# Optimization experiments

Measured on AMD Instinct MI355X. Metric: run time of the kernel, lower is better.

Reference implementation:

```python
import jax, jax.numpy as jnp
import numpy as np
from jax import lax

# STP parameters hard-coded in TFSTP.__init__ (stpPara)
U0 = 0.15        # u0
D_CONST = 0.05 * 20   # D = 1.0
F_CONST = 0.5 * 20    # F = 10.0
F_SMALL = 0.15        # f
R0 = 1.0


def _spike2interval(spk_bool):
    """Vectorized version of TFSTP.spike2interval.
    spk_bool: [T,H,W] bool. Returns isi [T,H,W] float32 with inf where undefined.
    For consecutive spikes s_k < s_{k+1}: isi[s_k+1 : s_{k+1}+1] = s_{k+1} - s_k.
    Equivalently isi[t] = next_spike_at_or_after(t) - last_spike_strictly_before(t).
    """
    T = spk_bool.shape[0]
    idx = jnp.arange(T, dtype=jnp.int32)[:, None, None]
    BIG = jnp.int32(T + 1)
    # last spike time <= t (running max of spike indices)
    prev_incl = lax.associative_scan(jnp.maximum, jnp.where(spk_bool, idx, -1), axis=0)
    # last spike time strictly < t (shift by one)
    prev_strict = jnp.concatenate(
        [jnp.full_like(prev_incl[:1], -1), prev_incl[:-1]], axis=0)
    # first spike time >= t (reverse running min)
    nxt = lax.associative_scan(jnp.minimum, jnp.where(spk_bool, idx, BIG),
                               axis=0, reverse=True)
    valid = (prev_strict >= 0) & (nxt < BIG)
    return jnp.where(valid, (nxt - prev_strict).astype(jnp.float32), jnp.inf)


def setup_inputs() -> dict:
    key = jax.random.key(0)
    T, H, W = 400, 250, 400
    spikes = jax.random.randint(key, (1, T, H, W), 0, 2).astype(jnp.float32)
    return {"spikes": spikes}


def reference(spikes):
    spk = spikes[0] > 0                    # [T,H,W] bool
    T, H, W = spk.shape
    half = T // 2                          # forward() breaks at t == T/2

    isi = _spike2interval(spk)             # [T,H,W]
    isi0 = isi[0]                          # prev_isi is fixed to intervals[0]

    R_init = jnp.full((H, W), R0, dtype=jnp.float32)
    u_init = jnp.full((H, W), U0, dtype=jnp.float32)

    def step(carry, xs):
        R, u = carry
        isi_t, spk_t = xs
        # update_idx = (isi_t != isi0) & (spk_t == 0) | (isi_t == 1)
        mask = ((isi_t != isi0) & (~spk_t)) | (isi_t == 1.0)
        exp_D = jnp.exp(-isi_t / D_CONST)   # exp(-inf)=0, discarded by mask
        exp_F = jnp.exp(-isi_t / F_CONST)
        R_new = jnp.where(mask, 1.0 - (1.0 - R * (1.0 - u)) * exp_D, R)
        u_new = jnp.where(mask, U0 + (u + F_SMALL * (1.0 - u) - U0) * exp_F, u)
        return (R_new, u_new), None

    # only the state at t = T//2 contributes to the output
    (R, u), _ = lax.scan(step, (R_init, u_init),
                         (isi[1:half + 1], spk[1:half + 1]))

    rho_u = -1.0 / (F_CONST * jnp.log(
        (u - U0) / (F_CONST - U0 + u * (1.0 - F_SMALL))))
    rho_R = -1.0 / (D_CONST * jnp.log(
        (1.0 - R) / (1.0 - R * (1.0 - u))))
    img = rho_u + rho_R

    mn, mx = img.min(), img.max()
    denom = jnp.where(mx == mn, 1.0, mx - mn)
    img = jnp.where(mx != mn, (img - mn) / denom, img)
    return img[None, None]  # [1,1,H,W]
```

## Files before the change

### kernel.cpp

```cpp
#include <hip/hip_runtime.h>
#include <math.h>

namespace {
constexpr int   T_STEPS = 400;
constexpr int   HALF    = 200;
constexpr int   NPIX    = 250 * 400;
constexpr int   CHUNK   = 32;
constexpr int   BLOCK   = 64;
constexpr int   NBLK    = (NPIX + BLOCK - 1) / BLOCK;
constexpr int   NORM_BLOCK = 256;
constexpr int   NORM_NBLK  = (NPIX + NORM_BLOCK - 1) / NORM_BLOCK;
constexpr float U0 = 0.15f;
}

__device__ __forceinline__ void apply_segment(float& R, float& u, int d, int n) {
  const float dd = (float)d;
  const float eD = expf(-dd);
  const float eF = expf(-(dd / 10.0f));
  for (int k = 0; k < n; ++k) {
    const float Rn = 1.0f - (1.0f - R * (1.0f - u)) * eD;
    const float un = U0 + (u + 0.15f * (1.0f - u) - U0) * eF;
    R = Rn; u = un;
  }
}

__device__ __forceinline__ void proc_mask(unsigned mask, int t0, int& prev,
                                          float& R, float& u, bool& done) {
  if (done) return;
  while (mask) {
    const int i = __builtin_ctz(mask);
    mask &= mask - 1u;
    const int t = t0 + i;
    if (prev >= 0) {
      const int d = t - prev;
      const int n = (t <= HALF) ? ((d == 1) ? 1 : (d - 1)) : (HALF - prev);
      apply_segment(R, u, d, n);
    }
    prev = t;
    if (t >= HALF) { done = true; return; }
  }
}

__global__ __launch_bounds__(BLOCK) void stp_compute(
    const float* __restrict__ spikes, float* __restrict__ img,
    float* __restrict__ pmin, float* __restrict__ pmax) {
  const int  p      = blockIdx.x * BLOCK + threadIdx.x;
  const bool active = (p < NPIX);
  const float* __restrict__ sp = spikes + (active ? p : (NPIX - 1));

  bool  done = !active;
  int   prev = -1;
  float R = 1.0f, u = U0;

  auto loadc = [&](float (&buf)[CHUNK], int c) {
#pragma unroll
    for (int i = 0; i < CHUNK; ++i) {
      const unsigned idx = (unsigned)(c * CHUNK + i) * (unsigned)NPIX;
      buf[i] = sp[idx];
    }
  };
  auto maskof = [&](const float (&buf)[CHUNK]) -> unsigned {
    unsigned m = 0u;
#pragma unroll
    for (int i = 0; i < CHUNK; ++i) m |= (buf[i] > 0.0f) ? (1u << i) : 0u;
    return m;
  };

  float va[CHUNK], vb[CHUNK];
  loadc(va, 0);
  loadc(vb, 1);
  unsigned m;
  m = maskof(va); loadc(va, 2); proc_mask(m, 0 * CHUNK, prev, R, u, done);
  m = maskof(vb); loadc(vb, 3); proc_mask(m, 1 * CHUNK, prev, R, u, done);
  m = maskof(va); loadc(va, 4); proc_mask(m, 2 * CHUNK, prev, R, u, done);
  m = maskof(vb); loadc(vb, 5); proc_mask(m, 3 * CHUNK, prev, R, u, done);
  m = maskof(va); loadc(va, 6); proc_mask(m, 4 * CHUNK, prev, R, u, done);
  m = maskof(vb);               proc_mask(m, 5 * CHUNK, prev, R, u, done);
  m = maskof(va);               proc_mask(m, 6 * CHUNK, prev, R, u, done);

  for (int c = 7; c <= (T_STEPS - 1) / CHUNK; ++c) {
    if (__all((int)done)) break;
    unsigned mt = 0u;
#pragma unroll
    for (int i = 0; i < CHUNK; ++i) {
      const int t = c * CHUNK + i;
      float v = 0.0f;
      if (t < T_STEPS) v = sp[(unsigned)t * (unsigned)NPIX];
      mt |= (v > 0.0f) ? (1u << i) : 0u;
    }
    proc_mask(mt, c * CHUNK, prev, R, u, done);
  }

  float val = 0.0f;
  if (active) {
    const float lu = logf((u - U0) / (10.0f - U0 + u * 0.85f));
    const float lR = logf((1.0f - R) / (1.0f - R * (1.0f - u)));
    val = (-1.0f / (10.0f * lu)) + (-1.0f / lR);
    img[p] = val;
  }

  float vmin = active ? val : INFINITY;
  float vmax = active ? val : -INFINITY;
#pragma unroll
  for (int off = 32; off > 0; off >>= 1) {
    vmin = fminf(vmin, __shfl_down(vmin, off, 64));
    vmax = fmaxf(vmax, __shfl_down(vmax, off, 64));
  }
  if (threadIdx.x == 0) {
    pmin[blockIdx.x] = vmin;
    pmax[blockIdx.x] = vmax;
  }
}

__global__ __launch_bounds__(512) void reduce_minmax(
    const float* __restrict__ pmin, const float* __restrict__ pmax,
    float* __restrict__ mm) {
  float vmin = INFINITY, vmax = -INFINITY;
  for (int i = threadIdx.x; i < NBLK; i += 512) {
    vmin = fminf(vmin, pmin[i]);
    vmax = fmaxf(vmax, pmax[i]);
  }
#pragma unroll
  for (int off = 32; off > 0; off >>= 1) {
    vmin = fminf(vmin, __shfl_down(vmin, off, 64));
    vmax = fmaxf(vmax, __shfl_down(vmax, off, 64));
  }
  __shared__ float smin[8], smax[8];
  const int lane = threadIdx.x & 63, wid = threadIdx.x >> 6;
  if (lane == 0) { smin[wid] = vmin; smax[wid] = vmax; }
  __syncthreads();
  if (threadIdx.x == 0) {
    float mn = smin[0], mx = smax[0];
#pragma unroll
    for (int i = 1; i < 8; ++i) {
      mn = fminf(mn, smin[i]);
      mx = fmaxf(mx, smax[i]);
    }
    mm[0] = mn;
    mm[1] = mx;
  }
}

__global__ __launch_bounds__(NORM_BLOCK) void normalize_k(
    float* __restrict__ img, const float* __restrict__ mm) {
  const int p = blockIdx.x * NORM_BLOCK + threadIdx.x;
  if (p < NPIX) {
    const float mn = mm[0], mx = mm[1];
    const float v  = img[p];
    img[p] = (mx != mn) ? (v - mn) / (mx - mn) : v;
  }
}

extern "C" void kernel_launch(void* const* d_in, const int* in_sizes, int n_in,
                              void* d_out, int out_size, void* d_ws, size_t ws_size,
                              hipStream_t stream) {
  const float* spikes = (const float*)d_in[0];
  float* out  = (float*)d_out;
  float* ws   = (float*)d_ws;
  float* mm   = ws;
  float* pmin = ws + 2;
  float* pmax = ws + 2 + NBLK;

  hipLaunchKernelGGL(stp_compute, dim3(NBLK), dim3(BLOCK), 0, stream,
                     spikes, out, pmin, pmax);
  hipLaunchKernelGGL(reduce_minmax, dim3(1), dim3(512), 0, stream,
                     pmin, pmax, mm);
  hipLaunchKernelGGL(normalize_k, dim3(NORM_NBLK), dim3(NORM_BLOCK), 0, stream,
                     out, mm);
}
```

Measured before the change: 84.44 us.

## Pre-pack spike bits in a wide parallel pass and fold min/max into atomics

Adds a separate kernel that reads the first 224 timesteps with float4 loads across a wide 2D grid and packs them into 32-bit spike masks. The recurrence kernel then reads seven words per pixel instead of streaming 224 floats, and falls back to raw float loads only for pixels that have not yet finished. The single-block min/max reduction kernel is replaced by per-block atomicMin/atomicMax on order-preserving integer keys, which removes one launch. In exchange, all 224 timesteps are always read during packing, even for pixels that would have stopped early, and there is extra global write traffic plus atomic contention.

```diff
diff --git a/kernel.cpp b/kernel.cpp
--- a/kernel.cpp
+++ b/kernel.cpp
@@ -5,12 +5,59 @@
 constexpr int   T_STEPS = 400;
 constexpr int   HALF    = 200;
 constexpr int   NPIX    = 250 * 400;
-constexpr int   CHUNK   = 32;
-constexpr int   BLOCK   = 64;
-constexpr int   NBLK    = (NPIX + BLOCK - 1) / BLOCK;
-constexpr int   NORM_BLOCK = 256;
-constexpr int   NORM_NBLK  = (NPIX + NORM_BLOCK - 1) / NORM_BLOCK;
+constexpr int   NWORDS  = 7;
+constexpr int   PRE_BLOCK   = 256;
+constexpr int   PXPT        = 8;
+constexpr int   PRE_THREADS = NPIX / PXPT;
+constexpr int   PRE_NBLK    = (PRE_THREADS + PRE_BLOCK - 1) / PRE_BLOCK;
+constexpr int   REC_BLOCK   = 64;
+constexpr int   REC_NBLK    = (NPIX + REC_BLOCK - 1) / REC_BLOCK;
+constexpr int   NORM_BLOCK  = 256;
+constexpr int   NORM_NBLK   = (NPIX + NORM_BLOCK - 1) / NORM_BLOCK;
 constexpr float U0 = 0.15f;
+}
+
+__device__ __forceinline__ unsigned fkey(float f) {
+  const unsigned u = __float_as_uint(f);
+  return (u & 0x80000000u) ? ~u : (u | 0x80000000u);
+}
+__device__ __forceinline__ float funkey(unsigned k) {
+  const unsigned u = (k & 0x80000000u) ? (k ^ 0x80000000u) : ~k;
+  return __uint_as_float(u);
+}
+
+__global__ __launch_bounds__(PRE_BLOCK) void pack_spikes(
+    const float* __restrict__ spikes, unsigned* __restrict__ packed,
+    unsigned* __restrict__ mm) {
+  if (blockIdx.x == 0 && blockIdx.y == 0 && threadIdx.x == 0) {
+    mm[0] = 0xFFFFFFFFu;
+    mm[1] = 0u;
+  }
+  const int tid = blockIdx.x * PRE_BLOCK + threadIdx.x;
+  if (tid >= PRE_THREADS) return;
+  const int w  = blockIdx.y;
+  const int px = tid * PXPT;
+
+  unsigned wb[PXPT] = {0u, 0u, 0u, 0u, 0u, 0u, 0u, 0u};
+  const size_t rowstart = (size_t)(w * 32) * NPIX + px;
+#pragma unroll 8
+  for (int t = 0; t < 32; ++t) {
+    const float4* rp = reinterpret_cast<const float4*>(spikes + rowstart + (size_t)t * NPIX);
+    const float4 a = rp[0];
+    const float4 b = rp[1];
+    const unsigned bit = 1u << t;
+    wb[0] |= (a.x > 0.0f) ? bit : 0u;
+    wb[1] |= (a.y > 0.0f) ? bit : 0u;
+    wb[2] |= (a.z > 0.0f) ? bit : 0u;
+    wb[3] |= (a.w > 0.0f) ? bit : 0u;
+    wb[4] |= (b.x > 0.0f) ? bit : 0u;
+    wb[5] |= (b.y > 0.0f) ? bit : 0u;
+    wb[6] |= (b.z > 0.0f) ? bit : 0u;
+    wb[7] |= (b.w > 0.0f) ? bit : 0u;
+  }
+  uint4* op = reinterpret_cast<uint4*>(packed + (size_t)w * NPIX + px);
+  op[0] = make_uint4(wb[0], wb[1], wb[2], wb[3]);
+  op[1] = make_uint4(wb[4], wb[5], wb[6], wb[7]);
 }
 
 __device__ __forceinline__ void apply_segment(float& R, float& u, int d, int n) {
@@ -41,54 +88,34 @@
   }
 }
 
-__global__ __launch_bounds__(BLOCK) void stp_compute(
-    const float* __restrict__ spikes, float* __restrict__ img,
-    float* __restrict__ pmin, float* __restrict__ pmax) {
-  const int  p      = blockIdx.x * BLOCK + threadIdx.x;
+__global__ __launch_bounds__(REC_BLOCK) void stp_recur(
+    const unsigned* __restrict__ packed, const float* __restrict__ spikes,
+    float* __restrict__ img, unsigned* __restrict__ mm) {
+  const int  p      = blockIdx.x * REC_BLOCK + threadIdx.x;
   const bool active = (p < NPIX);
-  const float* __restrict__ sp = spikes + (active ? p : (NPIX - 1));
+  const int  pc     = active ? p : (NPIX - 1);
 
   bool  done = !active;
   int   prev = -1;
   float R = 1.0f, u = U0;
 
-  auto loadc = [&](float (&buf)[CHUNK], int c) {
+  unsigned mw[NWORDS];
 #pragma unroll
-    for (int i = 0; i < CHUNK; ++i) {
-      const unsigned idx = (unsigned)(c * CHUNK + i) * (unsigned)NPIX;
-      buf[i] = sp[idx];
+  for (int w = 0; w < NWORDS; ++w) mw[w] = packed[(size_t)w * NPIX + pc];
+#pragma unroll
+  for (int w = 0; w < NWORDS; ++w) proc_mask(mw[w], w * 32, prev, R, u, done);
+
+  if (__any(done ? 0 : 1)) {
+    const float* spt = spikes + pc;
+    for (int t = NWORDS * 32; t < T_STEPS; ++t) {
+      if (__all(done ? 1 : 0)) break;
+      const float v = spt[(size_t)t * NPIX];
+      if (!done && v > 0.0f) {
+        if (prev >= 0) apply_segment(R, u, t - prev, HALF - prev);
+        prev = t;
+        done = true;
+      }
     }
-  };
-  auto maskof = [&](const float (&buf)[CHUNK]) -> unsigned {
-    unsigned m = 0u;
-#pragma unroll
-    for (int i = 0; i < CHUNK; ++i) m |= (buf[i] > 0.0f) ? (1u << i) : 0u;
-    return m;
-  };
-
-  float va[CHUNK], vb[CHUNK];
-  loadc(va, 0);
-  loadc(vb, 1);
-  unsigned m;
-  m = maskof(va); loadc(va, 2); proc_mask(m, 0 * CHUNK, prev, R, u, done);
-  m = maskof(vb); loadc(vb, 3); proc_mask(m, 1 * CHUNK, prev, R, u, done);
-  m = maskof(va); loadc(va, 4); proc_mask(m, 2 * CHUNK, prev, R, u, done);
-  m = maskof(vb); loadc(vb, 5); proc_mask(m, 3 * CHUNK, prev, R, u, done);
-  m = maskof(va); loadc(va, 6); proc_mask(m, 4 * CHUNK, prev, R, u, done);
-  m = maskof(vb);               proc_mask(m, 5 * CHUNK, prev, R, u, done);
-  m = maskof(va);               proc_mask(m, 6 * CHUNK, prev, R, u, done);
-
-  for (int c = 7; c <= (T_STEPS - 1) / CHUNK; ++c) {
-    if (__all((int)done)) break;
-    unsigned mt = 0u;
-#pragma unroll
-    for (int i = 0; i < CHUNK; ++i) {
-      const int t = c * CHUNK + i;
-      float v = 0.0f;
-      if (t < T_STEPS) v = sp[(unsigned)t * (unsigned)NPIX];
-      mt |= (v > 0.0f) ? (1u << i) : 0u;
-    }
-    proc_mask(mt, c * CHUNK, prev, R, u, done);
   }
 
   float val = 0.0f;
@@ -107,45 +134,17 @@
     vmax = fmaxf(vmax, __shfl_down(vmax, off, 64));
   }
   if (threadIdx.x == 0) {
-    pmin[blockIdx.x] = vmin;
-    pmax[blockIdx.x] = vmax;
-  }
-}
-
-__global__ __launch_bounds__(512) void reduce_minmax(
-    const float* __restrict__ pmin, const float* __restrict__ pmax,
-    float* __restrict__ mm) {
-  float vmin = INFINITY, vmax = -INFINITY;
-  for (int i = threadIdx.x; i < NBLK; i += 512) {
-    vmin = fminf(vmin, pmin[i]);
-    vmax = fmaxf(vmax, pmax[i]);
-  }
-#pragma unroll
-  for (int off = 32; off > 0; off >>= 1) {
-    vmin = fminf(vmin, __shfl_down(vmin, off, 64));
-    vmax = fmaxf(vmax, __shfl_down(vmax, off, 64));
-  }
-  __shared__ float smin[8], smax[8];
-  const int lane = threadIdx.x & 63, wid = threadIdx.x >> 6;
-  if (lane == 0) { smin[wid] = vmin; smax[wid] = vmax; }
-  __syncthreads();
-  if (threadIdx.x == 0) {
-    float mn = smin[0], mx = smax[0];
-#pragma unroll
-    for (int i = 1; i < 8; ++i) {
-      mn = fminf(mn, smin[i]);
-      mx = fmaxf(mx, smax[i]);
-    }
-    mm[0] = mn;
-    mm[1] = mx;
+    atomicMin(&mm[0], fkey(vmin));
+    atomicMax(&mm[1], fkey(vmax));
   }
 }
 
 __global__ __launch_bounds__(NORM_BLOCK) void normalize_k(
-    float* __restrict__ img, const float* __restrict__ mm) {
+    float* __restrict__ img, const unsigned* __restrict__ mm) {
   const int p = blockIdx.x * NORM_BLOCK + threadIdx.x;
   if (p < NPIX) {
-    const float mn = mm[0], mx = mm[1];
+    const float mn = funkey(mm[0]);
+    const float mx = funkey(mm[1]);
     const float v  = img[p];
     img[p] = (mx != mn) ? (v - mn) / (mx - mn) : v;
   }
@@ -155,16 +154,14 @@
                               void* d_out, int out_size, void* d_ws, size_t ws_size,
                               hipStream_t stream) {
   const float* spikes = (const float*)d_in[0];
-  float* out  = (float*)d_out;
-  float* ws   = (float*)d_ws;
-  float* mm   = ws;
-  float* pmin = ws + 2;
-  float* pmax = ws + 2 + NBLK;
+  float*    out    = (float*)d_out;
+  unsigned* mm     = (unsigned*)d_ws;
+  unsigned* packed = (unsigned*)d_ws + 64;
 
-  hipLaunchKernelGGL(stp_compute, dim3(NBLK), dim3(BLOCK), 0, stream,
-                     spikes, out, pmin, pmax);
-  hipLaunchKernelGGL(reduce_minmax, dim3(1), dim3(512), 0, stream,
-                     pmin, pmax, mm);
+  hipLaunchKernelGGL(pack_spikes, dim3(PRE_NBLK, NWORDS), dim3(PRE_BLOCK), 0, stream,
+                     spikes, packed, mm);
+  hipLaunchKernelGGL(stp_recur, dim3(REC_NBLK), dim3(REC_BLOCK), 0, stream,
+                     packed, spikes, out, mm);
   hipLaunchKernelGGL(normalize_k, dim3(NORM_NBLK), dim3(NORM_BLOCK), 0, stream,
                      out, mm);
 }
```

Measured after the change: 106.7 us. +26.4%, slower.

## Fuse min/max reduction and normalization into compute kernel with grid-wide atomic barrier

Applied to the files above, without the earlier changes.

Merges the three kernels into one. Each block folds its min/max into global atomics using order-preserving integer keys, bumps a counter, and spins until all blocks have arrived, then normalizes its own pixels directly. This removes two kernel launches and the write-then-reread of the image, and adds two small memsets. The spin barrier assumes all 1563 blocks are resident at once, which risks deadlock if occupancy is too low, and the launch bound is raised to ask for at least two waves per SIMD.

```diff
diff --git a/kernel.cpp b/kernel.cpp
--- a/kernel.cpp
+++ b/kernel.cpp
@@ -8,9 +8,16 @@
 constexpr int   CHUNK   = 32;
 constexpr int   BLOCK   = 64;
 constexpr int   NBLK    = (NPIX + BLOCK - 1) / BLOCK;
-constexpr int   NORM_BLOCK = 256;
-constexpr int   NORM_NBLK  = (NPIX + NORM_BLOCK - 1) / NORM_BLOCK;
 constexpr float U0 = 0.15f;
+}
+
+__device__ __forceinline__ unsigned fkey(float f) {
+  const unsigned u = __float_as_uint(f);
+  return (u & 0x80000000u) ? ~u : (u | 0x80000000u);
+}
+__device__ __forceinline__ float funkey(unsigned k) {
+  const unsigned u = (k & 0x80000000u) ? (k ^ 0x80000000u) : ~k;
+  return __uint_as_float(u);
 }
 
 __device__ __forceinline__ void apply_segment(float& R, float& u, int d, int n) {
@@ -41,9 +48,9 @@
   }
 }
 
-__global__ __launch_bounds__(BLOCK) void stp_compute(
+__global__ __launch_bounds__(BLOCK, 2) void stp_fused(
     const float* __restrict__ spikes, float* __restrict__ img,
-    float* __restrict__ pmin, float* __restrict__ pmax) {
+    unsigned* __restrict__ mm, unsigned* __restrict__ sync_ctr) {
   const int  p      = blockIdx.x * BLOCK + threadIdx.x;
   const bool active = (p < NPIX);
   const float* __restrict__ sp = spikes + (active ? p : (NPIX - 1));
@@ -79,7 +86,7 @@
   m = maskof(va);               proc_mask(m, 6 * CHUNK, prev, R, u, done);
 
   for (int c = 7; c <= (T_STEPS - 1) / CHUNK; ++c) {
-    if (__all((int)done)) break;
+    if (__all(done ? 1 : 0)) break;
     unsigned mt = 0u;
 #pragma unroll
     for (int i = 0; i < CHUNK; ++i) {
@@ -96,7 +103,6 @@
     const float lu = logf((u - U0) / (10.0f - U0 + u * 0.85f));
     const float lR = logf((1.0f - R) / (1.0f - R * (1.0f - u)));
     val = (-1.0f / (10.0f * lu)) + (-1.0f / lR);
-    img[p] = val;
   }
 
   float vmin = active ? val : INFINITY;
@@ -107,47 +113,23 @@
     vmax = fmaxf(vmax, __shfl_down(vmax, off, 64));
   }
   if (threadIdx.x == 0) {
-    pmin[blockIdx.x] = vmin;
-    pmax[blockIdx.x] = vmax;
+    atomicMin(&mm[0], fkey(vmin));
+    atomicMax(&mm[1], fkey(vmax));
+    __hip_atomic_fetch_add(&sync_ctr[0], 1u, __ATOMIC_RELEASE,
+                           __HIP_MEMORY_SCOPE_AGENT);
   }
-}
 
-__global__ __launch_bounds__(512) void reduce_minmax(
-    const float* __restrict__ pmin, const float* __restrict__ pmax,
-    float* __restrict__ mm) {
-  float vmin = INFINITY, vmax = -INFINITY;
-  for (int i = threadIdx.x; i < NBLK; i += 512) {
-    vmin = fminf(vmin, pmin[i]);
-    vmax = fmaxf(vmax, pmax[i]);
+  while (__hip_atomic_load(&sync_ctr[0], __ATOMIC_ACQUIRE,
+                           __HIP_MEMORY_SCOPE_AGENT) < (unsigned)NBLK) {
+    __builtin_amdgcn_s_sleep(8);
   }
-#pragma unroll
-  for (int off = 32; off > 0; off >>= 1) {
-    vmin = fminf(vmin, __shfl_down(vmin, off, 64));
-    vmax = fmaxf(vmax, __shfl_down(vmax, off, 64));
-  }
-  __shared__ float smin[8], smax[8];
-  const int lane = threadIdx.x & 63, wid = threadIdx.x >> 6;
-  if (lane == 0) { smin[wid] = vmin; smax[wid] = vmax; }
-  __syncthreads();
-  if (threadIdx.x == 0) {
-    float mn = smin[0], mx = smax[0];
-#pragma unroll
-    for (int i = 1; i < 8; ++i) {
-      mn = fminf(mn, smin[i]);
-      mx = fmaxf(mx, smax[i]);
-    }
-    mm[0] = mn;
-    mm[1] = mx;
-  }
-}
 
-__global__ __launch_bounds__(NORM_BLOCK) void normalize_k(
-    float* __restrict__ img, const float* __restrict__ mm) {
-  const int p = blockIdx.x * NORM_BLOCK + threadIdx.x;
-  if (p < NPIX) {
-    const float mn = mm[0], mx = mm[1];
-    const float v  = img[p];
-    img[p] = (mx != mn) ? (v - mn) / (mx - mn) : v;
+  const float mn = funkey(__hip_atomic_load(&mm[0], __ATOMIC_RELAXED,
+                                            __HIP_MEMORY_SCOPE_AGENT));
+  const float mx = funkey(__hip_atomic_load(&mm[1], __ATOMIC_RELAXED,
+                                            __HIP_MEMORY_SCOPE_AGENT));
+  if (active) {
+    img[p] = (mx != mn) ? (val - mn) / (mx - mn) : val;
   }
 }
 
@@ -155,16 +137,13 @@
                               void* d_out, int out_size, void* d_ws, size_t ws_size,
                               hipStream_t stream) {
   const float* spikes = (const float*)d_in[0];
-  float* out  = (float*)d_out;
-  float* ws   = (float*)d_ws;
-  float* mm   = ws;
-  float* pmin = ws + 2;
-  float* pmax = ws + 2 + NBLK;
+  float*    out = (float*)d_out;
+  unsigned* mm  = (unsigned*)d_ws;
+  unsigned* syn = (unsigned*)d_ws + 2;
 
-  hipLaunchKernelGGL(stp_compute, dim3(NBLK), dim3(BLOCK), 0, stream,
-                     spikes, out, pmin, pmax);
-  hipLaunchKernelGGL(reduce_minmax, dim3(1), dim3(512), 0, stream,
-                     pmin, pmax, mm);
-  hipLaunchKernelGGL(normalize_k, dim3(NORM_NBLK), dim3(NORM_BLOCK), 0, stream,
-                     out, mm);
+  hipMemsetAsync(mm, 0xFF, 4, stream);
+  hipMemsetAsync(mm + 1, 0x00, 8, stream);
+
+  hipLaunchKernelGGL(stp_fused, dim3(NBLK), dim3(BLOCK), 0, stream,
+                     spikes, out, mm, syn);
 }
```

Result: slower. 230.6 us (+173.1%).
